# Performance work log

Measured on AMD Instinct MI355X. Metric: run time of the kernel, lower is better.

Reference implementation:

```python
import jax, jax.numpy as jnp
import numpy as np
import math

L = 1024      # sequence length (residues)
E = 768       # hidden dim
P = 128       # pairwise state dim
H = 16        # heads
HD = E // H   # head width = 48
DEPTH = 8
MLP = 4 * E
FREQ = 256    # timestep frequency embedding size


def setup_inputs() -> dict:
    key = jax.random.key(0)
    ks = jax.random.split(key, 16)
    n = lambda i, shape, s=0.02: jax.random.normal(ks[i], shape, dtype=jnp.float32) * s
    return {
        'z': jax.random.normal(ks[0], (L, E), dtype=jnp.float32),
        't': jax.random.uniform(ks[1], (1,), dtype=jnp.float32),
        'bias': jax.random.normal(ks[2], (L, L, P), dtype=jnp.float32),
        'p2s_ln_g': jnp.ones((P,), jnp.float32),
        'p2s_ln_b': jnp.zeros((P,), jnp.float32),
        'p2s_w': n(3, (H, P)),
        't0_w': n(4, (E, FREQ)), 't0_b': jnp.zeros((E,), jnp.float32),
        't2_w': n(5, (E, E)), 't2_b': jnp.zeros((E,), jnp.float32),
        'blk_proj_w': n(6, (DEPTH, 3 * E, E)),
        'blk_o_w': n(7, (DEPTH, E, E)), 'blk_o_b': jnp.zeros((DEPTH, E), jnp.float32),
        'blk_ada_w': n(8, (DEPTH, 6 * E, E)), 'blk_ada_b': jnp.zeros((DEPTH, 6 * E), jnp.float32),
        'blk_fc1_w': n(9, (DEPTH, MLP, E)), 'blk_fc1_b': jnp.zeros((DEPTH, MLP), jnp.float32),
        'blk_fc2_w': n(10, (DEPTH, E, MLP)), 'blk_fc2_b': jnp.zeros((DEPTH, E), jnp.float32),
        'fin_ada_w': n(11, (2 * E, E)), 'fin_ada_b': jnp.zeros((2 * E,), jnp.float32),
        'fin_w': n(12, (E, E)), 'fin_b': jnp.zeros((E,), jnp.float32),
    }


def _ln(x, eps=1e-6):
    m = jnp.mean(x, axis=-1, keepdims=True)
    v = jnp.mean(jnp.square(x - m), axis=-1, keepdims=True)
    return (x - m) * jax.lax.rsqrt(v + eps)


def _mod(x, shift, scale):
    # x: [B,L,E]; shift/scale: [B,E]
    return x * (1.0 + scale[:, None, :]) + shift[:, None, :]


def _forward(z, t, bias, p2s_ln_g, p2s_ln_b, p2s_w, t0_w, t0_b, t2_w, t2_b,
             blk_proj_w, blk_o_w, blk_o_b, blk_ada_w, blk_ada_b,
             blk_fc1_w, blk_fc1_b, blk_fc2_w, blk_fc2_b,
             fin_ada_w, fin_ada_b, fin_w, fin_b):
    x = z[None]  # [1,L,E]
    # PairToSequence: LN (affine) + linear to per-head bias, laid out [B,H,Lq,Lk]
    b = _ln(bias[None]) * p2s_ln_g + p2s_ln_b        # [1,L,L,P]
    bh = jnp.einsum('blmp,hp->bhlm', b, p2s_w)       # [1,H,L,L]
    # TimestepEmbedder: sinusoidal -> MLP
    half = FREQ // 2
    freqs = jnp.exp(-math.log(10000.0) * jnp.arange(half, dtype=jnp.float32) / half)
    args = t[:, None] * freqs                        # [1,half]
    emb = jnp.concatenate([jnp.cos(args), jnp.sin(args)], axis=-1)  # [1,FREQ]
    c = jax.nn.silu(emb @ t0_w.T + t0_b) @ t2_w.T + t2_b            # [1,E]
    cs = jax.nn.silu(c)
    scale = HD ** -0.5

    def block(x, p):
        pw, ow, ob, aw, ab, f1w, f1b, f2w, f2b = p
        ada = cs @ aw.T + ab                         # [1,6E]
        sh1, sc1, g1, sh2, sc2, g2 = jnp.split(ada, 6, axis=1)
        h = _mod(_ln(x), sh1, sc1)
        # qkv: torch layout is (h, 3*hd) per token, chunk(3,-1) -> q,k,v
        qkv = (h @ pw.T).reshape(1, L, H, 3, HD)
        q = qkv[..., 0, :] * scale
        k = qkv[..., 1, :]
        v = qkv[..., 2, :]
        a = jnp.einsum('blhc,bmhc->bhlm', q, k) + bh  # full LxL scores + bias
        a = jax.nn.softmax(a, axis=-1)
        y = jnp.einsum('bhlm,bmhc->blhc', a, v).reshape(1, L, E)
        y = y @ ow.T + ob
        x = x + g1[:, None, :] * y
        h2 = _mod(_ln(x), sh2, sc2)
        h2 = jax.nn.gelu(h2 @ f1w.T + f1b, approximate=True) @ f2w.T + f2b
        return x + g2[:, None, :] * h2, None

    x, _ = jax.lax.scan(block, x, (blk_proj_w, blk_o_w, blk_o_b, blk_ada_w,
                                   blk_ada_b, blk_fc1_w, blk_fc1_b,
                                   blk_fc2_w, blk_fc2_b))
    ada = cs @ fin_ada_w.T + fin_ada_b               # [1,2E]
    sh, sc = jnp.split(ada, 2, axis=1)
    out = _mod(_ln(x), sh, sc) @ fin_w.T + fin_b
    return out[0]                                    # [L,E]


def reference(z, t, bias, p2s_ln_g, p2s_ln_b, p2s_w, t0_w, t0_b, t2_w, t2_b,
              blk_proj_w, blk_o_w, blk_o_b, blk_ada_w, blk_ada_b,
              blk_fc1_w, blk_fc1_b, blk_fc2_w, blk_fc2_b,
              fin_ada_w, fin_ada_b, fin_w, fin_b):
    return _forward(z, t, bias, p2s_ln_g, p2s_ln_b, p2s_w, t0_w, t0_b, t2_w,
                    t2_b, blk_proj_w, blk_o_w, blk_o_b, blk_ada_w, blk_ada_b,
                    blk_fc1_w, blk_fc1_b, blk_fc2_w, blk_fc2_b,
                    fin_ada_w, fin_ada_b, fin_w, fin_b)
```

## Files before the change

### kernel.cpp

```cpp
#include <hip/hip_runtime.h>
#include <hip/hip_bf16.h>
#include <math.h>

typedef unsigned short u16;
typedef unsigned int u32;
typedef __attribute__((ext_vector_type(8))) short bf16x8_t;
typedef __attribute__((ext_vector_type(4))) float f32x4_t;

constexpr int SEQ = 1024;
constexpr int EMB = 768;
constexpr int PDIM = 128;
constexpr int NH = 16;
constexpr int HDIM = 48;
constexpr int DMLP = 3072;
constexpr int NFREQ = 256;

__device__ __forceinline__ float bf2f(u16 h) {
  union { u32 u; float f; } v; v.u = ((u32)h) << 16; return v.f;
}
__device__ __forceinline__ u16 f2bf(float f) {
  union { float f; u32 u; } v; v.f = f;
  u32 r = v.u + 0x7fffu + ((v.u >> 16) & 1u);
  return (u16)(r >> 16);
}
__device__ __forceinline__ u32 pack_bf2(float lo, float hi) {
  return (u32)f2bf(lo) | ((u32)f2bf(hi) << 16);
}
__device__ __forceinline__ float silu_f(float x) { return x / (1.f + expf(-x)); }
__device__ __forceinline__ float gelu_t(float x) {
  float x3 = x * x * x;
  return 0.5f * x * (1.f + tanhf(0.7978845608028654f * (x + 0.044715f * x3)));
}

__global__ __launch_bounds__(256) void time1_kernel(
    const float* __restrict__ t, const float* __restrict__ t0_w,
    const float* __restrict__ t0_b, float* __restrict__ c1) {
  int e = (blockIdx.x * 256 + threadIdx.x) >> 6;
  int lane = threadIdx.x & 63;
  float tv = t[0];
  float acc = 0.f;
#pragma unroll
  for (int j = 0; j < 4; j++) {
    int i = lane + j * 64;
    int ii = (i < 128) ? i : (i - 128);
    float fr = expf(-9.210340371976184f * (float)ii / 128.f);
    float a = tv * fr;
    float ev = (i < 128) ? cosf(a) : sinf(a);
    acc += ev * t0_w[(long)e * NFREQ + i];
  }
#pragma unroll
  for (int m = 1; m < 64; m <<= 1) acc += __shfl_xor(acc, m, 64);
  if (lane == 0) {
    float s = acc + t0_b[e];
    c1[e] = silu_f(s);
  }
}

__global__ __launch_bounds__(256) void time2_kernel(
    const float* __restrict__ c1, const float* __restrict__ t2_w,
    const float* __restrict__ t2_b, float* __restrict__ cs) {
  int e = (blockIdx.x * 256 + threadIdx.x) >> 6;
  int lane = threadIdx.x & 63;
  float acc = 0.f;
#pragma unroll
  for (int j = 0; j < 12; j++)
    acc += c1[lane + j * 64] * t2_w[(long)e * EMB + lane + j * 64];
#pragma unroll
  for (int m = 1; m < 64; m <<= 1) acc += __shfl_xor(acc, m, 64);
  if (lane == 0) {
    float s = acc + t2_b[e];
    cs[e] = silu_f(s);
  }
}

__global__ __launch_bounds__(256) void ada_kernel(
    const float* __restrict__ cs,
    const float* __restrict__ blk_w, const float* __restrict__ blk_b,
    const float* __restrict__ fin_w, const float* __restrict__ fin_b,
    float* __restrict__ adas) {
  int r = (blockIdx.x * 256 + threadIdx.x) >> 6;
  int lane = threadIdx.x & 63;
  const float* wr = (r < 36864) ? (blk_w + (long)r * EMB)
                                : (fin_w + (long)(r - 36864) * EMB);
  float acc = 0.f;
#pragma unroll
  for (int j = 0; j < 12; j++)
    acc += cs[lane + j * 64] * wr[lane + j * 64];
#pragma unroll
  for (int m = 1; m < 64; m <<= 1) acc += __shfl_xor(acc, m, 64);
  if (lane == 0) {
    float b = (r < 36864) ? blk_b[r] : fin_b[r - 36864];
    adas[r] = acc + b;
  }
}

__global__ __launch_bounds__(256) void bias_bh_kernel(
    const float* __restrict__ bias, const float* __restrict__ gam,
    const float* __restrict__ bet, const float* __restrict__ w,
    u16* __restrict__ bh) {
  const int lane = threadIdx.x & 63;
  const int fm = lane & 15;
  const int fq = lane >> 4;

  bf16x8_t bfrag[4];
  float S = 0.f, T = 0.f;
#pragma unroll
  for (int t = 0; t < 4; t++) {
    int k0 = t * 32 + fq * 8;
    float4 w0 = *(const float4*)(w + fm * PDIM + k0);
    float4 w1 = *(const float4*)(w + fm * PDIM + k0 + 4);
    float4 g0 = *(const float4*)(gam + k0);
    float4 g1 = *(const float4*)(gam + k0 + 4);
    float4 e0 = *(const float4*)(bet + k0);
    float4 e1 = *(const float4*)(bet + k0 + 4);
    float wg[8] = {w0.x * g0.x, w0.y * g0.y, w0.z * g0.z, w0.w * g0.w,
                   w1.x * g1.x, w1.y * g1.y, w1.z * g1.z, w1.w * g1.w};
    S += wg[0] + wg[1] + wg[2] + wg[3] + wg[4] + wg[5] + wg[6] + wg[7];
    T += w0.x * e0.x + w0.y * e0.y + w0.z * e0.z + w0.w * e0.w +
         w1.x * e1.x + w1.y * e1.y + w1.z * e1.z + w1.w * e1.w;
    union { bf16x8_t f; u32 u[4]; } bu;
#pragma unroll
    for (int i = 0; i < 4; i++) bu.u[i] = pack_bf2(wg[2 * i], wg[2 * i + 1]);
    bfrag[t] = bu.f;
  }
  S += __shfl_xor(S, 16, 64); S += __shfl_xor(S, 32, 64);
  T += __shfl_xor(T, 16, 64); T += __shfl_xor(T, 32, 64);

  const long ngroup = (long)SEQ * SEQ / 16;
  const long nwave = (long)gridDim.x * 4;
  long gw = ((long)blockIdx.x * 256 + threadIdx.x) >> 6;
  for (long grp = gw; grp < ngroup; grp += nwave) {
    const float* bp = bias + grp * (16 * PDIM) + (long)fm * PDIM;
    float v[32];
#pragma unroll
    for (int t = 0; t < 4; t++) {
      float4 a0 = *(const float4*)(bp + t * 32 + fq * 8);
      float4 a1 = *(const float4*)(bp + t * 32 + fq * 8 + 4);
      v[t * 8 + 0] = a0.x; v[t * 8 + 1] = a0.y; v[t * 8 + 2] = a0.z; v[t * 8 + 3] = a0.w;
      v[t * 8 + 4] = a1.x; v[t * 8 + 5] = a1.y; v[t * 8 + 6] = a1.z; v[t * 8 + 7] = a1.w;
    }
    float s = 0.f, ss = 0.f;
#pragma unroll
    for (int i = 0; i < 32; i++) { s += v[i]; ss += v[i] * v[i]; }
    s += __shfl_xor(s, 16, 64); s += __shfl_xor(s, 32, 64);
    ss += __shfl_xor(ss, 16, 64); ss += __shfl_xor(ss, 32, 64);

    f32x4_t acc = {};
#pragma unroll
    for (int t = 0; t < 4; t++) {
      union { bf16x8_t f; u32 u[4]; } au;
#pragma unroll
      for (int i = 0; i < 4; i++)
        au.u[i] = pack_bf2(v[t * 8 + 2 * i], v[t * 8 + 2 * i + 1]);
      acc = __builtin_amdgcn_mfma_f32_16x16x32_bf16(au.f, bfrag[t], acc, 0, 0, 0);
    }
    long pbase = grp * 16;
#pragma unroll
    for (int r = 0; r < 4; r++) {
      int p = fq * 4 + r;
      float sp = __shfl(s, p, 64);
      float ssp = __shfl(ss, p, 64);
      float mu = sp * (1.f / PDIM);
      float rr = rsqrtf(ssp * (1.f / PDIM) - mu * mu + 1e-6f);
      float out = rr * (acc[r] - mu * S) + T;
      bh[(long)fm * SEQ * SEQ + pbase + p] = f2bf(out);
    }
  }
}

__global__ __launch_bounds__(256) void cvt4_kernel(
    const float* __restrict__ s0, int n0, const float* __restrict__ s1, int n1,
    const float* __restrict__ s2, int n2, const float* __restrict__ s3, int n3,
    u16* __restrict__ dst) {
  long total = ((long)n0 + n1 + n2 + n3) >> 2;
  for (long i = (long)blockIdx.x * 256 + threadIdx.x; i < total;
       i += (long)gridDim.x * 256) {
    long e = i << 2;
    const float* s; long off;
    if (e < n0) { s = s0; off = e; }
    else if (e < (long)n0 + n1) { s = s1; off = e - n0; }
    else if (e < (long)n0 + n1 + n2) { s = s2; off = e - n0 - n1; }
    else { s = s3; off = e - n0 - n1 - n2; }
    float4 v = *(const float4*)(s + off);
    ushort4 o;
    o.x = f2bf(v.x); o.y = f2bf(v.y); o.z = f2bf(v.z); o.w = f2bf(v.w);
    *(ushort4*)(dst + e) = o;
  }
}

__global__ __launch_bounds__(256) void ln_mod_kernel(
    const float* __restrict__ x, const float* __restrict__ sh,
    const float* __restrict__ sc, u16* __restrict__ out) {
  int row = blockIdx.x * 4 + (threadIdx.x >> 6);
  int lane = threadIdx.x & 63;
  const float* xr = x + (long)row * EMB;
  float4 xv[3];
  float s = 0.f, ss = 0.f;
#pragma unroll
  for (int j = 0; j < 3; j++) {
    xv[j] = *(const float4*)(xr + j * 256 + lane * 4);
    s += xv[j].x + xv[j].y + xv[j].z + xv[j].w;
    ss += xv[j].x * xv[j].x + xv[j].y * xv[j].y + xv[j].z * xv[j].z + xv[j].w * xv[j].w;
  }
#pragma unroll
  for (int m = 1; m < 64; m <<= 1) {
    s += __shfl_xor(s, m, 64);
    ss += __shfl_xor(ss, m, 64);
  }
  float mu = s * (1.f / EMB);
  float r = rsqrtf(ss * (1.f / EMB) - mu * mu + 1e-6f);
#pragma unroll
  for (int j = 0; j < 3; j++) {
    int c = j * 256 + lane * 4;
    float4 shv = *(const float4*)(sh + c);
    float4 scv = *(const float4*)(sc + c);
    ushort4 o;
    o.x = f2bf((xv[j].x - mu) * r * (1.f + scv.x) + shv.x);
    o.y = f2bf((xv[j].y - mu) * r * (1.f + scv.y) + shv.y);
    o.z = f2bf((xv[j].z - mu) * r * (1.f + scv.z) + shv.z);
    o.w = f2bf((xv[j].w - mu) * r * (1.f + scv.w) + shv.w);
    *(ushort4*)(out + (long)row * EMB + c) = o;
  }
}

__global__ __launch_bounds__(256) void softmax_kernel(u16* __restrict__ sp) {
  long row = (long)blockIdx.x * 4 + (threadIdx.x >> 6);
  int lane = threadIdx.x & 63;
  u16* p = sp + row * SEQ;
  uint4 u0 = *(uint4*)(p + lane * 8);
  uint4 u1 = *(uint4*)(p + 512 + lane * 8);
  float v[16];
  u32 uu[8] = {u0.x, u0.y, u0.z, u0.w, u1.x, u1.y, u1.z, u1.w};
#pragma unroll
  for (int i = 0; i < 8; i++) {
    v[2 * i] = bf2f((u16)(uu[i] & 0xffffu));
    v[2 * i + 1] = bf2f((u16)(uu[i] >> 16));
  }
  float mx = v[0];
#pragma unroll
  for (int i = 1; i < 16; i++) mx = fmaxf(mx, v[i]);
#pragma unroll
  for (int m = 1; m < 64; m <<= 1) mx = fmaxf(mx, __shfl_xor(mx, m, 64));
  float sum = 0.f;
#pragma unroll
  for (int i = 0; i < 16; i++) {
    v[i] = expf(v[i] - mx);
    sum += v[i];
  }
#pragma unroll
  for (int m = 1; m < 64; m <<= 1) sum += __shfl_xor(sum, m, 64);
  float inv = 1.f / sum;
#pragma unroll
  for (int i = 0; i < 8; i++)
    uu[i] = (u32)f2bf(v[2 * i] * inv) | ((u32)f2bf(v[2 * i + 1] * inv) << 16);
  *(uint4*)(p + lane * 8) = make_uint4(uu[0], uu[1], uu[2], uu[3]);
  *(uint4*)(p + 512 + lane * 8) = make_uint4(uu[4], uu[5], uu[6], uu[7]);
}

enum { M_PLAIN, M_QKV, M_LOGITS, M_PV, M_RESID, M_GELU };

template <int MODE>
__global__ __launch_bounds__(256) void gemm_bt_kernel(
    const u16* __restrict__ A, long sAz, int lda,
    const u16* __restrict__ Bt, long sBz, int ldb,
    int M, int N, int K,
    const float* __restrict__ bias, const float* __restrict__ gate,
    const u16* __restrict__ addb,
    float* __restrict__ outf, int ldo,
    u16* __restrict__ outb, long sObz, int ldob,
    u16* __restrict__ qout, u16* __restrict__ kout, u16* __restrict__ vtout,
    float qscale) {
  __shared__ __align__(16) u16 As[64][40];
  __shared__ __align__(16) u16 Bs[64][40];
  const int tid = threadIdx.x;
  const int lane = tid & 63, wid = tid >> 6;
  const int bm = blockIdx.y * 64, bn = blockIdx.x * 64;
  const int z = blockIdx.z;
  const u16* Ab = A + (long)z * sAz;
  const u16* Bb = Bt + (long)z * sBz;
  const int ar = tid >> 2, ac = (tid & 3) * 8;
  const int wm = (wid >> 1) * 32, wn = (wid & 1) * 32;
  const int fm = lane & 15, fq = lane >> 4;
  f32x4_t acc[2][2] = {};
  for (int k0 = 0; k0 < K; k0 += 32) {
    uint4 av = make_uint4(0, 0, 0, 0);
    if (k0 + ac < K)
      av = *(const uint4*)(Ab + (long)(bm + ar) * lda + (k0 + ac));
    *(uint4*)(&As[ar][ac]) = av;
    uint4 bv = make_uint4(0, 0, 0, 0);
    if ((bn + ar) < N && (k0 + ac) < K)
      bv = *(const uint4*)(Bb + (long)(bn + ar) * ldb + (k0 + ac));
    *(uint4*)(&Bs[ar][ac]) = bv;
    __syncthreads();
    bf16x8_t a0 = *(const bf16x8_t*)(&As[wm + fm][fq * 8]);
    bf16x8_t a1 = *(const bf16x8_t*)(&As[wm + 16 + fm][fq * 8]);
    bf16x8_t b0 = *(const bf16x8_t*)(&Bs[wn + fm][fq * 8]);
    bf16x8_t b1 = *(const bf16x8_t*)(&Bs[wn + 16 + fm][fq * 8]);
    acc[0][0] = __builtin_amdgcn_mfma_f32_16x16x32_bf16(a0, b0, acc[0][0], 0, 0, 0);
    acc[0][1] = __builtin_amdgcn_mfma_f32_16x16x32_bf16(a0, b1, acc[0][1], 0, 0, 0);
    acc[1][0] = __builtin_amdgcn_mfma_f32_16x16x32_bf16(a1, b0, acc[1][0], 0, 0, 0);
    acc[1][1] = __builtin_amdgcn_mfma_f32_16x16x32_bf16(a1, b1, acc[1][1], 0, 0, 0);
    __syncthreads();
  }
#pragma unroll
  for (int mf = 0; mf < 2; mf++)
#pragma unroll
    for (int nf = 0; nf < 2; nf++) {
      int col = bn + wn + nf * 16 + fm;
      if (col >= N) continue;
      int hh = 0, tt = 0, cc = 0;
      if constexpr (MODE == M_QKV) {
        hh = col / (3 * HDIM);
        int rr = col - hh * 3 * HDIM;
        tt = rr / HDIM;
        cc = rr - tt * HDIM;
      }
#pragma unroll
      for (int r = 0; r < 4; r++) {
        int row = bm + wm + mf * 16 + fq * 4 + r;
        float v = acc[mf][nf][r];
        if constexpr (MODE == M_PLAIN) {
          outf[(long)row * ldo + col] = v + bias[col];
        } else if constexpr (MODE == M_QKV) {
          if (tt == 0)
            qout[(long)hh * SEQ * HDIM + (long)row * HDIM + cc] = f2bf(v * qscale);
          else if (tt == 1)
            kout[(long)hh * SEQ * HDIM + (long)row * HDIM + cc] = f2bf(v);
          else
            vtout[(long)hh * HDIM * SEQ + (long)cc * SEQ + row] = f2bf(v);
        } else if constexpr (MODE == M_LOGITS) {
          long idx = (long)z * sObz + (long)row * ldob + col;
          outb[idx] = f2bf(v + bf2f(addb[idx]));
        } else if constexpr (MODE == M_PV) {
          outb[(long)row * ldob + z * HDIM + col] = f2bf(v);
        } else if constexpr (MODE == M_RESID) {
          long idx = (long)row * ldo + col;
          outf[idx] = outf[idx] + gate[col] * (v + bias[col]);
        } else if constexpr (MODE == M_GELU) {
          outb[(long)row * ldob + col] = f2bf(gelu_t(v + bias[col]));
        }
      }
    }
}

extern "C" void kernel_launch(void* const* d_in, const int* in_sizes, int n_in,
                              void* d_out, int out_size, void* d_ws, size_t ws_size,
                              hipStream_t stream) {
  const float* z = (const float*)d_in[0];
  const float* t = (const float*)d_in[1];
  const float* bias = (const float*)d_in[2];
  const float* p2s_ln_g = (const float*)d_in[3];
  const float* p2s_ln_b = (const float*)d_in[4];
  const float* p2s_w = (const float*)d_in[5];
  const float* t0_w = (const float*)d_in[6];
  const float* t0_b = (const float*)d_in[7];
  const float* t2_w = (const float*)d_in[8];
  const float* t2_b = (const float*)d_in[9];
  const float* blk_proj_w = (const float*)d_in[10];
  const float* blk_o_w = (const float*)d_in[11];
  const float* blk_o_b = (const float*)d_in[12];
  const float* blk_ada_w = (const float*)d_in[13];
  const float* blk_ada_b = (const float*)d_in[14];
  const float* blk_fc1_w = (const float*)d_in[15];
  const float* blk_fc1_b = (const float*)d_in[16];
  const float* blk_fc2_w = (const float*)d_in[17];
  const float* blk_fc2_b = (const float*)d_in[18];
  const float* fin_ada_w = (const float*)d_in[19];
  const float* fin_ada_b = (const float*)d_in[20];
  const float* fin_w = (const float*)d_in[21];
  const float* fin_b = (const float*)d_in[22];

  char* base = (char*)d_ws;
  size_t off = 0;
  auto alloc = [&](size_t bytes) {
    void* p = base + off;
    off += (bytes + 255) & ~(size_t)255;
    return p;
  };
  float* x = (float*)alloc((size_t)SEQ * EMB * 4);
  float* c1 = (float*)alloc(EMB * 4);
  float* cs = (float*)alloc(EMB * 4);
  float* adas = (float*)alloc(38400 * 4);
  u16* hbuf = (u16*)alloc((size_t)SEQ * EMB * 2);
  u16* qb = (u16*)alloc((size_t)NH * SEQ * HDIM * 2);
  u16* kb = (u16*)alloc((size_t)NH * SEQ * HDIM * 2);
  u16* vtb = (u16*)alloc((size_t)NH * SEQ * HDIM * 2);
  u16* y2 = (u16*)alloc((size_t)SEQ * EMB * 2);
  u16* mlp = (u16*)alloc((size_t)SEQ * DMLP * 2);
  u16* bh = (u16*)alloc((size_t)NH * SEQ * SEQ * 2);
  u16* SP = (u16*)alloc((size_t)NH * SEQ * SEQ * 2);
  u16* wbuf = (u16*)alloc((size_t)7077888 * 2);
  u16* wfin = (u16*)alloc((size_t)589824 * 2);
  (void)ws_size; (void)in_sizes; (void)n_in; (void)out_size;

  hipMemcpyAsync(x, z, (size_t)SEQ * EMB * 4, hipMemcpyDeviceToDevice, stream);
  time1_kernel<<<192, 256, 0, stream>>>(t, t0_w, t0_b, c1);
  time2_kernel<<<192, 256, 0, stream>>>(c1, t2_w, t2_b, cs);
  ada_kernel<<<9600, 256, 0, stream>>>(cs, blk_ada_w, blk_ada_b, fin_ada_w, fin_ada_b, adas);
  bias_bh_kernel<<<1024, 256, 0, stream>>>(bias, p2s_ln_g, p2s_ln_b, p2s_w, bh);
  cvt4_kernel<<<576, 256, 0, stream>>>(fin_w, 589824, nullptr, 0, nullptr, 0, nullptr, 0, wfin);

  const float qscale = 1.0f / sqrtf((float)HDIM);
  const int owoff = 2304 * 768;
  const int f1off = owoff + 768 * 768;
  const int f2off = f1off + 3072 * 768;

  for (int d = 0; d < 8; d++) {
    const float* pw = blk_proj_w + (long)d * 2304 * 768;
    const float* ow = blk_o_w + (long)d * 768 * 768;
    const float* f1 = blk_fc1_w + (long)d * 3072 * 768;
    const float* f2 = blk_fc2_w + (long)d * 768 * 3072;
    cvt4_kernel<<<6912, 256, 0, stream>>>(pw, 2304 * 768, ow, 768 * 768,
                                          f1, 3072 * 768, f2, 768 * 3072, wbuf);
    const float* ada = adas + d * 4608;
    ln_mod_kernel<<<256, 256, 0, stream>>>(x, ada + 0, ada + 768, hbuf);
    gemm_bt_kernel<M_QKV><<<dim3(36, 16, 1), 256, 0, stream>>>(
        hbuf, 0, EMB, wbuf, 0, EMB, SEQ, 3 * EMB, EMB,
        nullptr, nullptr, nullptr, nullptr, 0, nullptr, 0, 0,
        qb, kb, vtb, qscale);
    gemm_bt_kernel<M_LOGITS><<<dim3(16, 16, 16), 256, 0, stream>>>(
        qb, (long)SEQ * HDIM, HDIM, kb, (long)SEQ * HDIM, HDIM, SEQ, SEQ, HDIM,
        nullptr, nullptr, bh, nullptr, 0, SP, (long)SEQ * SEQ, SEQ,
        nullptr, nullptr, nullptr, 0.f);
    softmax_kernel<<<4096, 256, 0, stream>>>(SP);
    gemm_bt_kernel<M_PV><<<dim3(1, 16, 16), 256, 0, stream>>>(
        SP, (long)SEQ * SEQ, SEQ, vtb, (long)HDIM * SEQ, SEQ, SEQ, HDIM, SEQ,
        nullptr, nullptr, nullptr, nullptr, 0, y2, 0, EMB,
        nullptr, nullptr, nullptr, 0.f);
    gemm_bt_kernel<M_RESID><<<dim3(12, 16, 1), 256, 0, stream>>>(
        y2, 0, EMB, wbuf + owoff, 0, EMB, SEQ, EMB, EMB,
        blk_o_b + d * EMB, ada + 1536, nullptr, x, EMB, nullptr, 0, 0,
        nullptr, nullptr, nullptr, 0.f);
    ln_mod_kernel<<<256, 256, 0, stream>>>(x, ada + 2304, ada + 3072, hbuf);
    gemm_bt_kernel<M_GELU><<<dim3(48, 16, 1), 256, 0, stream>>>(
        hbuf, 0, EMB, wbuf + f1off, 0, EMB, SEQ, DMLP, EMB,
        blk_fc1_b + d * DMLP, nullptr, nullptr, nullptr, 0, mlp, 0, DMLP,
        nullptr, nullptr, nullptr, 0.f);
    gemm_bt_kernel<M_RESID><<<dim3(12, 16, 1), 256, 0, stream>>>(
        mlp, 0, DMLP, wbuf + f2off, 0, DMLP, SEQ, EMB, DMLP,
        blk_fc2_b + d * EMB, ada + 3840, nullptr, x, EMB, nullptr, 0, 0,
        nullptr, nullptr, nullptr, 0.f);
  }
  ln_mod_kernel<<<256, 256, 0, stream>>>(x, adas + 36864, adas + 36864 + 768, hbuf);
  gemm_bt_kernel<M_PLAIN><<<dim3(12, 16, 1), 256, 0, stream>>>(
      hbuf, 0, EMB, wfin, 0, EMB, SEQ, EMB, EMB,
      fin_b, nullptr, nullptr, (float*)d_out, EMB, nullptr, 0, 0,
      nullptr, nullptr, nullptr, 0.f);
}
```

Before: 2.415 ms.

## Add 128x128-tile GEMM with direct-to-LDS loads and split-K atomics; convert weights once

Adds a new GEMM kernel with 128x128 block tiles and 64x64 per-wave tiles (4x4 MFMA fragments). It loads global data straight into LDS with global_load_lds, and splits K for the two residual projections, accumulating into the residual stream with atomicAdd. The QKV, o-proj, fc1, fc2 and final GEMMs move to this kernel. All block weights are now converted to bf16 in one launch before the layer loop instead of once per layer. The aim is more data reuse per tile, fewer launches and less instruction overhead for loading. In exchange it uses a larger workspace, makes the residual summation order nondeterministic through atomics, and runs a single-buffered loop with no prefetch.

Result: faster. 2.267 ms (-6.1%).

```diff
diff --git a/kernel.cpp b/kernel.cpp
--- a/kernel.cpp
+++ b/kernel.cpp
@@ -30,6 +30,12 @@
 __device__ __forceinline__ float gelu_t(float x) {
   float x3 = x * x * x;
   return 0.5f * x * (1.f + tanhf(0.7978845608028654f * (x + 0.044715f * x3)));
+}
+
+__device__ __forceinline__ void gload16(const u16* g, u16* l) {
+  __builtin_amdgcn_global_load_lds(
+      (__attribute__((address_space(1))) void*)(void*)g,
+      (__attribute__((address_space(3))) void*)l, 16, 0, 0);
 }
 
 __global__ __launch_bounds__(256) void time1_kernel(
@@ -308,39 +314,108 @@
     for (int nf = 0; nf < 2; nf++) {
       int col = bn + wn + nf * 16 + fm;
       if (col >= N) continue;
-      int hh = 0, tt = 0, cc = 0;
-      if constexpr (MODE == M_QKV) {
-        hh = col / (3 * HDIM);
-        int rr = col - hh * 3 * HDIM;
-        tt = rr / HDIM;
-        cc = rr - tt * HDIM;
-      }
 #pragma unroll
       for (int r = 0; r < 4; r++) {
         int row = bm + wm + mf * 16 + fq * 4 + r;
         float v = acc[mf][nf][r];
-        if constexpr (MODE == M_PLAIN) {
-          outf[(long)row * ldo + col] = v + bias[col];
-        } else if constexpr (MODE == M_QKV) {
+        if constexpr (MODE == M_LOGITS) {
+          long idx = (long)z * sObz + (long)row * ldob + col;
+          outb[idx] = f2bf(v + bf2f(addb[idx]));
+        } else if constexpr (MODE == M_PV) {
+          outb[(long)row * ldob + z * HDIM + col] = f2bf(v);
+        }
+      }
+    }
+}
+
+enum { G_PLAIN, G_QKV, G_RESID, G_GELU };
+
+template <int MODE>
+__global__ __launch_bounds__(256) void gemm128_kernel(
+    const u16* __restrict__ A, int lda,
+    const u16* __restrict__ Bt, int ldb, int K,
+    const float* __restrict__ bias, const float* __restrict__ gate,
+    float* __restrict__ outf, int ldo,
+    u16* __restrict__ outb, int ldob,
+    u16* __restrict__ qout, u16* __restrict__ kout, u16* __restrict__ vtout,
+    float qscale) {
+  __shared__ __align__(16) u16 smem[8192];
+  const int tid = threadIdx.x;
+  const int lane = tid & 63, wid = tid >> 6;
+  const int bm = blockIdx.y * 128, bn = blockIdx.x * 128;
+  const long koff = (long)blockIdx.z * K;
+  const int r0 = tid >> 2;
+  const int ce = (tid & 3) * 8;
+  const u16* gA0 = A + (long)(bm + r0) * lda + koff + ce;
+  const u16* gA1 = gA0 + (long)64 * lda;
+  const u16* gB0 = Bt + (long)(bn + r0) * ldb + koff + ce;
+  const u16* gB1 = gB0 + (long)64 * ldb;
+  u16* lA0 = &smem[r0 * 32 + ce];
+  u16* lA1 = lA0 + 64 * 32;
+  u16* lB0 = lA0 + 4096;
+  u16* lB1 = lB0 + 64 * 32;
+  const int wm = (wid >> 1) * 64, wn = (wid & 1) * 64;
+  const int fm = lane & 15, fq = lane >> 4;
+  const u16* pa = &smem[(wm + fm) * 32 + fq * 8];
+  const u16* pb = &smem[4096 + (wn + fm) * 32 + fq * 8];
+  f32x4_t acc[4][4] = {};
+  for (int k0 = 0; k0 < K; k0 += 32) {
+    gload16(gA0 + k0, lA0);
+    gload16(gA1 + k0, lA1);
+    gload16(gB0 + k0, lB0);
+    gload16(gB1 + k0, lB1);
+    __syncthreads();
+    bf16x8_t a[4], b[4];
+#pragma unroll
+    for (int i = 0; i < 4; i++) a[i] = *(const bf16x8_t*)(pa + i * 16 * 32);
+#pragma unroll
+    for (int i = 0; i < 4; i++) b[i] = *(const bf16x8_t*)(pb + i * 16 * 32);
+#pragma unroll
+    for (int mf = 0; mf < 4; mf++)
+#pragma unroll
+      for (int nf = 0; nf < 4; nf++)
+        acc[mf][nf] = __builtin_amdgcn_mfma_f32_16x16x32_bf16(a[mf], b[nf], acc[mf][nf], 0, 0, 0);
+    __syncthreads();
+  }
+#pragma unroll
+  for (int nf = 0; nf < 4; nf++) {
+    const int col = bn + wn + nf * 16 + fm;
+    int hh = 0, tt = 0, cc = 0;
+    if constexpr (MODE == G_QKV) {
+      hh = col / (3 * HDIM);
+      int rr2 = col - hh * 3 * HDIM;
+      tt = rr2 / HDIM;
+      cc = rr2 - tt * HDIM;
+    }
+    float bcol = 0.f, gcol = 0.f;
+    if constexpr (MODE == G_PLAIN || MODE == G_GELU) bcol = bias[col];
+    if constexpr (MODE == G_RESID) {
+      gcol = gate[col];
+      bcol = (blockIdx.z == 0) ? bias[col] : 0.f;
+    }
+#pragma unroll
+    for (int mf = 0; mf < 4; mf++) {
+#pragma unroll
+      for (int r = 0; r < 4; r++) {
+        const int row = bm + wm + mf * 16 + fq * 4 + r;
+        float v = acc[mf][nf][r];
+        if constexpr (MODE == G_PLAIN) {
+          outf[(long)row * ldo + col] = v + bcol;
+        } else if constexpr (MODE == G_QKV) {
           if (tt == 0)
             qout[(long)hh * SEQ * HDIM + (long)row * HDIM + cc] = f2bf(v * qscale);
           else if (tt == 1)
             kout[(long)hh * SEQ * HDIM + (long)row * HDIM + cc] = f2bf(v);
           else
             vtout[(long)hh * HDIM * SEQ + (long)cc * SEQ + row] = f2bf(v);
-        } else if constexpr (MODE == M_LOGITS) {
-          long idx = (long)z * sObz + (long)row * ldob + col;
-          outb[idx] = f2bf(v + bf2f(addb[idx]));
-        } else if constexpr (MODE == M_PV) {
-          outb[(long)row * ldob + z * HDIM + col] = f2bf(v);
-        } else if constexpr (MODE == M_RESID) {
-          long idx = (long)row * ldo + col;
-          outf[idx] = outf[idx] + gate[col] * (v + bias[col]);
-        } else if constexpr (MODE == M_GELU) {
-          outb[(long)row * ldob + col] = f2bf(gelu_t(v + bias[col]));
+        } else if constexpr (MODE == G_RESID) {
+          atomicAdd(&outf[(long)row * ldo + col], gcol * (v + bcol));
+        } else if constexpr (MODE == G_GELU) {
+          outb[(long)row * ldob + col] = f2bf(gelu_t(v + bcol));
         }
       }
     }
+  }
 }
 
 extern "C" void kernel_launch(void* const* d_in, const int* in_sizes, int n_in,
@@ -389,7 +464,7 @@
   u16* mlp = (u16*)alloc((size_t)SEQ * DMLP * 2);
   u16* bh = (u16*)alloc((size_t)NH * SEQ * SEQ * 2);
   u16* SP = (u16*)alloc((size_t)NH * SEQ * SEQ * 2);
-  u16* wbuf = (u16*)alloc((size_t)7077888 * 2);
+  u16* wball = (u16*)alloc((size_t)56623104 * 2);
   u16* wfin = (u16*)alloc((size_t)589824 * 2);
   (void)ws_size; (void)in_sizes; (void)n_in; (void)out_size;
 
@@ -398,25 +473,26 @@
   time2_kernel<<<192, 256, 0, stream>>>(c1, t2_w, t2_b, cs);
   ada_kernel<<<9600, 256, 0, stream>>>(cs, blk_ada_w, blk_ada_b, fin_ada_w, fin_ada_b, adas);
   bias_bh_kernel<<<1024, 256, 0, stream>>>(bias, p2s_ln_g, p2s_ln_b, p2s_w, bh);
+  cvt4_kernel<<<2048, 256, 0, stream>>>(blk_proj_w, 14155776, blk_o_w, 4718592,
+                                        blk_fc1_w, 18874368, blk_fc2_w, 18874368, wball);
   cvt4_kernel<<<576, 256, 0, stream>>>(fin_w, 589824, nullptr, 0, nullptr, 0, nullptr, 0, wfin);
 
   const float qscale = 1.0f / sqrtf((float)HDIM);
-  const int owoff = 2304 * 768;
-  const int f1off = owoff + 768 * 768;
-  const int f2off = f1off + 3072 * 768;
+  const long o_base = 14155776;
+  const long f1_base = 18874368;
+  const long f2_base = 37748736;
 
   for (int d = 0; d < 8; d++) {
-    const float* pw = blk_proj_w + (long)d * 2304 * 768;
-    const float* ow = blk_o_w + (long)d * 768 * 768;
-    const float* f1 = blk_fc1_w + (long)d * 3072 * 768;
-    const float* f2 = blk_fc2_w + (long)d * 768 * 3072;
-    cvt4_kernel<<<6912, 256, 0, stream>>>(pw, 2304 * 768, ow, 768 * 768,
-                                          f1, 3072 * 768, f2, 768 * 3072, wbuf);
+    const u16* pw = wball + (long)d * 2304 * 768;
+    const u16* ow = wball + o_base + (long)d * 768 * 768;
+    const u16* f1 = wball + f1_base + (long)d * 3072 * 768;
+    const u16* f2 = wball + f2_base + (long)d * 768 * 3072;
     const float* ada = adas + d * 4608;
+
     ln_mod_kernel<<<256, 256, 0, stream>>>(x, ada + 0, ada + 768, hbuf);
-    gemm_bt_kernel<M_QKV><<<dim3(36, 16, 1), 256, 0, stream>>>(
-        hbuf, 0, EMB, wbuf, 0, EMB, SEQ, 3 * EMB, EMB,
-        nullptr, nullptr, nullptr, nullptr, 0, nullptr, 0, 0,
+    gemm128_kernel<G_QKV><<<dim3(18, 8, 1), 256, 0, stream>>>(
+        hbuf, EMB, pw, EMB, EMB,
+        nullptr, nullptr, nullptr, 0, nullptr, 0,
         qb, kb, vtb, qscale);
     gemm_bt_kernel<M_LOGITS><<<dim3(16, 16, 16), 256, 0, stream>>>(
         qb, (long)SEQ * HDIM, HDIM, kb, (long)SEQ * HDIM, HDIM, SEQ, SEQ, HDIM,
@@ -427,23 +503,23 @@
         SP, (long)SEQ * SEQ, SEQ, vtb, (long)HDIM * SEQ, SEQ, SEQ, HDIM, SEQ,
         nullptr, nullptr, nullptr, nullptr, 0, y2, 0, EMB,
         nullptr, nullptr, nullptr, 0.f);
-    gemm_bt_kernel<M_RESID><<<dim3(12, 16, 1), 256, 0, stream>>>(
-        y2, 0, EMB, wbuf + owoff, 0, EMB, SEQ, EMB, EMB,
-        blk_o_b + d * EMB, ada + 1536, nullptr, x, EMB, nullptr, 0, 0,
+    gemm128_kernel<G_RESID><<<dim3(6, 8, 4), 256, 0, stream>>>(
+        y2, EMB, ow, EMB, 192,
+        blk_o_b + d * EMB, ada + 1536, x, EMB, nullptr, 0,
         nullptr, nullptr, nullptr, 0.f);
     ln_mod_kernel<<<256, 256, 0, stream>>>(x, ada + 2304, ada + 3072, hbuf);
-    gemm_bt_kernel<M_GELU><<<dim3(48, 16, 1), 256, 0, stream>>>(
-        hbuf, 0, EMB, wbuf + f1off, 0, EMB, SEQ, DMLP, EMB,
-        blk_fc1_b + d * DMLP, nullptr, nullptr, nullptr, 0, mlp, 0, DMLP,
+    gemm128_kernel<G_GELU><<<dim3(24, 8, 1), 256, 0, stream>>>(
+        hbuf, EMB, f1, EMB, EMB,
+        blk_fc1_b + d * DMLP, nullptr, nullptr, 0, mlp, DMLP,
         nullptr, nullptr, nullptr, 0.f);
-    gemm_bt_kernel<M_RESID><<<dim3(12, 16, 1), 256, 0, stream>>>(
-        mlp, 0, DMLP, wbuf + f2off, 0, DMLP, SEQ, EMB, DMLP,
-        blk_fc2_b + d * EMB, ada + 3840, nullptr, x, EMB, nullptr, 0, 0,
+    gemm128_kernel<G_RESID><<<dim3(6, 8, 4), 256, 0, stream>>>(
+        mlp, DMLP, f2, DMLP, 768,
+        blk_fc2_b + d * EMB, ada + 3840, x, EMB, nullptr, 0,
         nullptr, nullptr, nullptr, 0.f);
   }
   ln_mod_kernel<<<256, 256, 0, stream>>>(x, adas + 36864, adas + 36864 + 768, hbuf);
-  gemm_bt_kernel<M_PLAIN><<<dim3(12, 16, 1), 256, 0, stream>>>(
-      hbuf, 0, EMB, wfin, 0, EMB, SEQ, EMB, EMB,
-      fin_b, nullptr, nullptr, (float*)d_out, EMB, nullptr, 0, 0,
+  gemm128_kernel<G_PLAIN><<<dim3(6, 8, 1), 256, 0, stream>>>(
+      hbuf, EMB, wfin, EMB, EMB,
+      fin_b, nullptr, (float*)d_out, EMB, nullptr, 0,
       nullptr, nullptr, nullptr, 0.f);
 }
```
